# Optimization experiments

Measured on AMD Instinct MI355X. Metric: run time of the kernel, lower is better.

## Reference

```python
import jax, jax.numpy as jnp
import numpy as np

N_POINTS = 32768
N_PRIMS = 2048
C_LIGHT = 299792458.0


def setup_inputs() -> dict:
    key = jax.random.key(0)
    k1, k2, k3, k4, k5 = jax.random.split(key, 5)
    # query points and primitive centers in a ~room-scale scene (metres)
    query_points = jax.random.normal(k1, (N_POINTS, 3), dtype=jnp.float32) * 2.0
    positions = jax.random.normal(k2, (N_PRIMS, 3), dtype=jnp.float32) * 2.0
    # diagonal anisotropic scales, kept away from zero for stability
    scales = jax.random.uniform(k3, (N_PRIMS, 3), dtype=jnp.float32, minval=0.1, maxval=1.0)
    amplitudes = jax.random.uniform(k4, (N_PRIMS,), dtype=jnp.float32, minval=0.0, maxval=1.0)
    phases = jax.random.uniform(k5, (N_PRIMS,), dtype=jnp.float32, minval=-np.pi, maxval=np.pi)
    return {
        "query_points": query_points,
        "positions": positions,
        "scales": scales,
        "amplitudes": amplitudes,
        "phases": phases,
        "frequency": 2400000000,  # 2.4 GHz
    }


def reference(query_points, positions, scales, amplitudes, phases, frequency):
    """Batched equivalent of: field = sum_p primitive_p.evaluate(query_points, frequency).

    Each complex Gaussian primitive contributes
        a_p * exp(-0.5 * (x-mu_p)^T diag(1/s_p^2) (x-mu_p)) * exp(i*(phi_p + k*|x-mu_p|))
    with wavenumber k = 2*pi*f/c. All pairwise terms are expressed as GEMMs.
    """
    f = jnp.float32(frequency)
    k_wave = jnp.float32(2.0 * np.pi) * f / jnp.float32(C_LIGHT)

    inv_var = 1.0 / (scales * scales)                      # [P,3]
    x2 = query_points * query_points                       # [N,3]
    mu2w = jnp.sum(positions * positions * inv_var, axis=1)  # [P]
    # Mahalanobis distance^2: sum_d (x_d-mu_d)^2 / s_d^2, expanded into GEMMs
    maha = (x2 @ inv_var.T
            - 2.0 * (query_points @ (positions * inv_var).T)
            + mu2w[None, :])                               # [N,P]
    maha = jnp.maximum(maha, 0.0)
    # Euclidean distance for the propagation phase
    d2 = (jnp.sum(x2, axis=1, keepdims=True)
          - 2.0 * (query_points @ positions.T)
          + jnp.sum(positions * positions, axis=1)[None, :])  # [N,P]
    r = jnp.sqrt(jnp.maximum(d2, 1e-12))

    w = amplitudes[None, :] * jnp.exp(-0.5 * maha)         # [N,P] real envelope
    ph = phases[None, :] + k_wave * r                      # [N,P] total phase
    field = jax.lax.complex(jnp.sum(w * jnp.cos(ph), axis=1),
                            jnp.sum(w * jnp.sin(ph), axis=1))  # [N] complex64
    return field
```

## Files before the change

### kernel.cpp

```cpp
#include <hip/hip_runtime.h>
#include <math.h>

#define NPOINTS 32768
#define NPRIMS  2048
#define BLK     256

typedef float v2f __attribute__((ext_vector_type(2)));

struct PrimDup { float4 q0, q1, q2, q3; };

__device__ __forceinline__ float read_freq(const void* p) {
    const unsigned* w = (const unsigned*)p;
    unsigned lo = w[0];
    float ff = __uint_as_float(lo);
    if (ff >= 1.0e5f && ff <= 1.0e13f) return ff;
    if (lo != 0u) return (float)lo;
    double d = *(const double*)p;
    if (d >= 1.0e5 && d <= 1.0e13) return (float)d;
    unsigned long long v = ((unsigned long long)w[1] << 32) | lo;
    return (float)v;
}

__global__ __launch_bounds__(BLK) void prep_kernel(
        const float* __restrict__ pos,
        const float* __restrict__ scl,
        const float* __restrict__ amp,
        const float* __restrict__ ph,
        PrimDup* __restrict__ pd) {
    int p = blockIdx.x * blockDim.x + threadIdx.x;
    if (p >= NPRIMS) return;
    const float KE     = -0.72134752044448169f;
    const float INV2PI =  0.15915494309189535f;
    float sx = scl[3*p+0], sy = scl[3*p+1], sz = scl[3*p+2];
    float gx = KE / (sx*sx), gy = KE / (sy*sy), gz = KE / (sz*sz);
    float pr = ph[p] * INV2PI;
    PrimDup D;
    D.q0 = make_float4(pos[3*p+0], pos[3*p+0], pos[3*p+1], pos[3*p+1]);
    D.q1 = make_float4(pos[3*p+2], pos[3*p+2], amp[p], amp[p]);
    D.q2 = make_float4(gx, gx, gy, gy);
    D.q3 = make_float4(gz, gz, pr, pr);
    pd[p] = D;
}

template <int NSPLIT>
__global__ __launch_bounds__(BLK) void field_kernel(
        const float* __restrict__ qp,
        const PrimDup* __restrict__ pd,
        const void* __restrict__ freq_p,
        float2* __restrict__ part) {
    constexpr int PCOUNT = NPRIMS / NSPLIT;
    const int n0 = blockIdx.x * (BLK * 2) + threadIdx.x;
    const int n1 = n0 + BLK;
    const float kr = read_freq(freq_p) / 299792458.0f;
    const v2f kr2 = {kr, kr};

    const v2f xx = {qp[3*n0+0], qp[3*n1+0]};
    const v2f yy = {qp[3*n0+1], qp[3*n1+1]};
    const v2f zz = {qp[3*n0+2], qp[3*n1+2]};

    v2f re = {0.0f, 0.0f}, im = {0.0f, 0.0f};

    const int base = blockIdx.y * PCOUNT;
    #pragma unroll 4
    for (int j = 0; j < PCOUNT; ++j) {
        PrimDup D = pd[base + j];
        v2f mux = {D.q0.x, D.q0.y}, muy = {D.q0.z, D.q0.w};
        v2f muz = {D.q1.x, D.q1.y}, am2 = {D.q1.z, D.q1.w};
        v2f gx  = {D.q2.x, D.q2.y}, gy  = {D.q2.z, D.q2.w};
        v2f gz  = {D.q3.x, D.q3.y}, ph2 = {D.q3.z, D.q3.w};

        v2f dx = xx - mux, dy = yy - muy, dz = zz - muz;
        v2f t0 = dx * dx, t1 = dy * dy, t2 = dz * dz;
        v2f e  = t0 * gx + t1 * gy + t2 * gz;
        v2f d2 = t0 + t1 + t2;
        d2 = __builtin_elementwise_max(d2, (v2f){1e-12f, 1e-12f});

        v2f r2 = {__builtin_amdgcn_sqrtf(d2.x), __builtin_amdgcn_sqrtf(d2.y)};
        v2f ex = {__builtin_amdgcn_exp2f(e.x),  __builtin_amdgcn_exp2f(e.y)};
        v2f w2 = am2 * ex;
        v2f tp = __builtin_elementwise_fma(kr2, r2, ph2);
        float f0 = __builtin_amdgcn_fractf(tp.x);
        float f1 = __builtin_amdgcn_fractf(tp.y);
        v2f s2 = {__builtin_amdgcn_sinf(f0), __builtin_amdgcn_sinf(f1)};
        v2f c2 = {__builtin_amdgcn_cosf(f0), __builtin_amdgcn_cosf(f1)};
        re = __builtin_elementwise_fma(w2, c2, re);
        im = __builtin_elementwise_fma(w2, s2, im);
    }

    part[(size_t)blockIdx.y * NPOINTS + n0] = make_float2(re.x, im.x);
    part[(size_t)blockIdx.y * NPOINTS + n1] = make_float2(re.y, im.y);
}

template <int NSPLIT>
__global__ __launch_bounds__(BLK) void reduce_kernel(const float2* __restrict__ part,
                                                     float* __restrict__ out) {
    int n = blockIdx.x * blockDim.x + threadIdx.x;
    float re = 0.0f, im = 0.0f;
    #pragma unroll
    for (int s = 0; s < NSPLIT; ++s) {
        float2 v = part[(size_t)s * NPOINTS + n];
        re += v.x; im += v.y;
    }
    out[n]           = re;
    out[NPOINTS + n] = im;
}

__global__ __launch_bounds__(BLK) void field_fallback(
        const float* __restrict__ qp,
        const float* __restrict__ pos,
        const float* __restrict__ scl,
        const float* __restrict__ amp,
        const float* __restrict__ ph,
        const void*  __restrict__ freq_p,
        float*       __restrict__ out) {
    __shared__ float4 sA[128];
    __shared__ float4 sB[128];
    const int n = blockIdx.x * BLK + threadIdx.x;
    const float x = qp[3*n+0], y = qp[3*n+1], z = qp[3*n+2];
    const float kr = read_freq(freq_p) / 299792458.0f;
    const float KE = -0.72134752044448169f, INV2PI = 0.15915494309189535f;
    float re = 0.0f, im = 0.0f;
    for (int tile = 0; tile < NPRIMS / 128; ++tile) {
        __syncthreads();
        if (threadIdx.x < 128) {
            int p = tile * 128 + threadIdx.x;
            float sx = scl[3*p+0], sy = scl[3*p+1], sz = scl[3*p+2];
            sA[threadIdx.x] = make_float4(pos[3*p+0], pos[3*p+1], pos[3*p+2], amp[p]);
            sB[threadIdx.x] = make_float4(KE/(sx*sx), KE/(sy*sy), KE/(sz*sz), ph[p]*INV2PI);
        }
        __syncthreads();
        #pragma unroll 8
        for (int p = 0; p < 128; ++p) {
            float4 a = sA[p];
            float4 b = sB[p];
            float dx = x - a.x, dy = y - a.y, dz = z - a.z;
            float t0 = dx*dx, t1 = dy*dy, t2 = dz*dz;
            float e  = fmaf(t0, b.x, fmaf(t1, b.y, t2 * b.z));
            float d2 = t0 + t1 + t2;
            float r  = __builtin_amdgcn_sqrtf(fmaxf(d2, 1e-12f));
            float w  = a.w * __builtin_amdgcn_exp2f(e);
            float tp = __builtin_amdgcn_fractf(fmaf(kr, r, b.w));
            float s  = __builtin_amdgcn_sinf(tp);
            float c  = __builtin_amdgcn_cosf(tp);
            re = fmaf(w, c, re);
            im = fmaf(w, s, im);
        }
    }
    out[n]           = re;
    out[NPOINTS + n] = im;
}

extern "C" void kernel_launch(void* const* d_in, const int* in_sizes, int n_in,
                              void* d_out, int out_size, void* d_ws, size_t ws_size,
                              hipStream_t stream) {
    const float* qp  = (const float*)d_in[0];
    const float* pos = (const float*)d_in[1];
    const float* scl = (const float*)d_in[2];
    const float* amp = (const float*)d_in[3];
    const float* ph  = (const float*)d_in[4];
    const void*  fq  = d_in[5];
    float* out = (float*)d_out;

    const size_t packed_bytes = (size_t)NPRIMS * sizeof(PrimDup);
    const size_t ps32 = packed_bytes + (size_t)32 * NPOINTS * sizeof(float2);
    const size_t ps16 = packed_bytes + (size_t)16 * NPOINTS * sizeof(float2);

    if (ws_size >= ps32) {
        PrimDup* pd   = (PrimDup*)d_ws;
        float2*  part = (float2*)((char*)d_ws + packed_bytes);
        prep_kernel<<<dim3(NPRIMS / BLK), dim3(BLK), 0, stream>>>(pos, scl, amp, ph, pd);
        field_kernel<32><<<dim3(NPOINTS / (BLK * 2), 32), dim3(BLK), 0, stream>>>(qp, pd, fq, part);
        reduce_kernel<32><<<dim3(NPOINTS / BLK), dim3(BLK), 0, stream>>>(part, out);
    } else if (ws_size >= ps16) {
        PrimDup* pd   = (PrimDup*)d_ws;
        float2*  part = (float2*)((char*)d_ws + packed_bytes);
        prep_kernel<<<dim3(NPRIMS / BLK), dim3(BLK), 0, stream>>>(pos, scl, amp, ph, pd);
        field_kernel<16><<<dim3(NPOINTS / (BLK * 2), 16), dim3(BLK), 0, stream>>>(qp, pd, fq, part);
        reduce_kernel<16><<<dim3(NPOINTS / BLK), dim3(BLK), 0, stream>>>(part, out);
    } else {
        field_fallback<<<dim3(NPOINTS / BLK), dim3(BLK), 0, stream>>>(qp, pos, scl, amp, ph, fq, out);
    }
}
```

Measured before the change: 50.74 us.

## Process four points per thread and split primitives 64 ways

Each thread now evaluates two packed point pairs, so every loaded primitive record is reused across four query points instead of two. The primitive dimension is split into 64 chunks instead of 32 to keep the grid size constant. In exchange, the partial-sum buffer and the reduction pass double in size, and the path needs a larger workspace.

```diff
diff --git a/kernel.cpp b/kernel.cpp
--- a/kernel.cpp
+++ b/kernel.cpp
@@ -42,26 +42,31 @@
     pd[p] = D;
 }
 
-template <int NSPLIT>
+template <int NSPLIT, int NPAIR>
 __global__ __launch_bounds__(BLK) void field_kernel(
         const float* __restrict__ qp,
         const PrimDup* __restrict__ pd,
         const void* __restrict__ freq_p,
         float2* __restrict__ part) {
     constexpr int PCOUNT = NPRIMS / NSPLIT;
-    const int n0 = blockIdx.x * (BLK * 2) + threadIdx.x;
-    const int n1 = n0 + BLK;
+    const int n0 = blockIdx.x * (BLK * 2 * NPAIR) + threadIdx.x;
     const float kr = read_freq(freq_p) / 299792458.0f;
     const v2f kr2 = {kr, kr};
 
-    const v2f xx = {qp[3*n0+0], qp[3*n1+0]};
-    const v2f yy = {qp[3*n0+1], qp[3*n1+1]};
-    const v2f zz = {qp[3*n0+2], qp[3*n1+2]};
-
-    v2f re = {0.0f, 0.0f}, im = {0.0f, 0.0f};
+    v2f xx[NPAIR], yy[NPAIR], zz[NPAIR], re[NPAIR], im[NPAIR];
+    #pragma unroll
+    for (int i = 0; i < NPAIR; ++i) {
+        int a = n0 + (2 * i) * BLK;
+        int b = n0 + (2 * i + 1) * BLK;
+        xx[i] = (v2f){qp[3*a+0], qp[3*b+0]};
+        yy[i] = (v2f){qp[3*a+1], qp[3*b+1]};
+        zz[i] = (v2f){qp[3*a+2], qp[3*b+2]};
+        re[i] = (v2f){0.0f, 0.0f};
+        im[i] = (v2f){0.0f, 0.0f};
+    }
 
     const int base = blockIdx.y * PCOUNT;
-    #pragma unroll 4
+    #pragma unroll 2
     for (int j = 0; j < PCOUNT; ++j) {
         PrimDup D = pd[base + j];
         v2f mux = {D.q0.x, D.q0.y}, muy = {D.q0.z, D.q0.w};
@@ -69,26 +74,34 @@
         v2f gx  = {D.q2.x, D.q2.y}, gy  = {D.q2.z, D.q2.w};
         v2f gz  = {D.q3.x, D.q3.y}, ph2 = {D.q3.z, D.q3.w};
 
-        v2f dx = xx - mux, dy = yy - muy, dz = zz - muz;
-        v2f t0 = dx * dx, t1 = dy * dy, t2 = dz * dz;
-        v2f e  = t0 * gx + t1 * gy + t2 * gz;
-        v2f d2 = t0 + t1 + t2;
-        d2 = __builtin_elementwise_max(d2, (v2f){1e-12f, 1e-12f});
+        #pragma unroll
+        for (int i = 0; i < NPAIR; ++i) {
+            v2f dx = xx[i] - mux, dy = yy[i] - muy, dz = zz[i] - muz;
+            v2f t0 = dx * dx, t1 = dy * dy, t2 = dz * dz;
+            v2f e  = t0 * gx + t1 * gy + t2 * gz;
+            v2f d2 = t0 + t1 + t2;
+            d2 = __builtin_elementwise_max(d2, (v2f){1e-12f, 1e-12f});
 
-        v2f r2 = {__builtin_amdgcn_sqrtf(d2.x), __builtin_amdgcn_sqrtf(d2.y)};
-        v2f ex = {__builtin_amdgcn_exp2f(e.x),  __builtin_amdgcn_exp2f(e.y)};
-        v2f w2 = am2 * ex;
-        v2f tp = __builtin_elementwise_fma(kr2, r2, ph2);
-        float f0 = __builtin_amdgcn_fractf(tp.x);
-        float f1 = __builtin_amdgcn_fractf(tp.y);
-        v2f s2 = {__builtin_amdgcn_sinf(f0), __builtin_amdgcn_sinf(f1)};
-        v2f c2 = {__builtin_amdgcn_cosf(f0), __builtin_amdgcn_cosf(f1)};
-        re = __builtin_elementwise_fma(w2, c2, re);
-        im = __builtin_elementwise_fma(w2, s2, im);
+            v2f r2 = {__builtin_amdgcn_sqrtf(d2.x), __builtin_amdgcn_sqrtf(d2.y)};
+            v2f ex = {__builtin_amdgcn_exp2f(e.x),  __builtin_amdgcn_exp2f(e.y)};
+            v2f w2 = am2 * ex;
+            v2f tp = __builtin_elementwise_fma(kr2, r2, ph2);
+            float f0 = __builtin_amdgcn_fractf(tp.x);
+            float f1 = __builtin_amdgcn_fractf(tp.y);
+            v2f s2 = {__builtin_amdgcn_sinf(f0), __builtin_amdgcn_sinf(f1)};
+            v2f c2 = {__builtin_amdgcn_cosf(f0), __builtin_amdgcn_cosf(f1)};
+            re[i] = __builtin_elementwise_fma(w2, c2, re[i]);
+            im[i] = __builtin_elementwise_fma(w2, s2, im[i]);
+        }
     }
 
-    part[(size_t)blockIdx.y * NPOINTS + n0] = make_float2(re.x, im.x);
-    part[(size_t)blockIdx.y * NPOINTS + n1] = make_float2(re.y, im.y);
+    #pragma unroll
+    for (int i = 0; i < NPAIR; ++i) {
+        int a = n0 + (2 * i) * BLK;
+        int b = n0 + (2 * i + 1) * BLK;
+        part[(size_t)blockIdx.y * NPOINTS + a] = make_float2(re[i].x, im[i].x);
+        part[(size_t)blockIdx.y * NPOINTS + b] = make_float2(re[i].y, im[i].y);
+    }
 }
 
 template <int NSPLIT>
@@ -162,21 +175,21 @@
     float* out = (float*)d_out;
 
     const size_t packed_bytes = (size_t)NPRIMS * sizeof(PrimDup);
+    const size_t ps64 = packed_bytes + (size_t)64 * NPOINTS * sizeof(float2);
     const size_t ps32 = packed_bytes + (size_t)32 * NPOINTS * sizeof(float2);
-    const size_t ps16 = packed_bytes + (size_t)16 * NPOINTS * sizeof(float2);
 
-    if (ws_size >= ps32) {
+    if (ws_size >= ps64) {
         PrimDup* pd   = (PrimDup*)d_ws;
         float2*  part = (float2*)((char*)d_ws + packed_bytes);
         prep_kernel<<<dim3(NPRIMS / BLK), dim3(BLK), 0, stream>>>(pos, scl, amp, ph, pd);
-        field_kernel<32><<<dim3(NPOINTS / (BLK * 2), 32), dim3(BLK), 0, stream>>>(qp, pd, fq, part);
-        reduce_kernel<32><<<dim3(NPOINTS / BLK), dim3(BLK), 0, stream>>>(part, out);
-    } else if (ws_size >= ps16) {
+        field_kernel<64, 2><<<dim3(NPOINTS / (BLK * 4), 64), dim3(BLK), 0, stream>>>(qp, pd, fq, part);
+        reduce_kernel<64><<<dim3(NPOINTS / BLK), dim3(BLK), 0, stream>>>(part, out);
+    } else if (ws_size >= ps32) {
         PrimDup* pd   = (PrimDup*)d_ws;
         float2*  part = (float2*)((char*)d_ws + packed_bytes);
         prep_kernel<<<dim3(NPRIMS / BLK), dim3(BLK), 0, stream>>>(pos, scl, amp, ph, pd);
-        field_kernel<16><<<dim3(NPOINTS / (BLK * 2), 16), dim3(BLK), 0, stream>>>(qp, pd, fq, part);
-        reduce_kernel<16><<<dim3(NPOINTS / BLK), dim3(BLK), 0, stream>>>(part, out);
+        field_kernel<32, 1><<<dim3(NPOINTS / (BLK * 2), 32), dim3(BLK), 0, stream>>>(qp, pd, fq, part);
+        reduce_kernel<32><<<dim3(NPOINTS / BLK), dim3(BLK), 0, stream>>>(part, out);
     } else {
         field_fallback<<<dim3(NPOINTS / BLK), dim3(BLK), 0, stream>>>(qp, pos, scl, amp, ph, fq, out);
     }
```

New measurement: 55.85 us. +10.1%, slower.

## Spatially sort query points and cull negligible Gaussian primitives per wavefront

Applied to the files above, without the earlier changes.

Adds a Morton-cell binning pipeline (histogram, scan, scatter) that reorders query points so each wavefront covers a compact region. In the field kernel each wavefront computes a bounding box of its points and skips any primitive whose Gaussian exponent over that box is provably below 2^-21. Skipped primitives contribute at most that tiny relative weight, so the heavy transcendental work drops for distant primitives. The cost is five extra small kernel launches, atomics, an indirect scatter on output, and a small approximation error.

```diff
diff --git a/kernel.cpp b/kernel.cpp
--- a/kernel.cpp
+++ b/kernel.cpp
@@ -4,6 +4,7 @@
 #define NPOINTS 32768
 #define NPRIMS  2048
 #define BLK     256
+#define NCELLS  4096
 
 typedef float v2f __attribute__((ext_vector_type(2)));
 
@@ -22,44 +23,174 @@
 }
 
 __global__ __launch_bounds__(BLK) void prep_kernel(
-        const float* __restrict__ pos,
-        const float* __restrict__ scl,
-        const float* __restrict__ amp,
-        const float* __restrict__ ph,
+        const float* __restrict__ pos, const float* __restrict__ scl,
+        const float* __restrict__ amp, const float* __restrict__ ph,
         PrimDup* __restrict__ pd) {
     int p = blockIdx.x * blockDim.x + threadIdx.x;
     if (p >= NPRIMS) return;
-    const float KE     = -0.72134752044448169f;
-    const float INV2PI =  0.15915494309189535f;
+    const float KE = -0.72134752044448169f, INV2PI = 0.15915494309189535f;
     float sx = scl[3*p+0], sy = scl[3*p+1], sz = scl[3*p+2];
-    float gx = KE / (sx*sx), gy = KE / (sy*sy), gz = KE / (sz*sz);
-    float pr = ph[p] * INV2PI;
     PrimDup D;
     D.q0 = make_float4(pos[3*p+0], pos[3*p+0], pos[3*p+1], pos[3*p+1]);
     D.q1 = make_float4(pos[3*p+2], pos[3*p+2], amp[p], amp[p]);
-    D.q2 = make_float4(gx, gx, gy, gy);
-    D.q3 = make_float4(gz, gz, pr, pr);
+    D.q2 = make_float4(KE/(sx*sx), KE/(sx*sx), KE/(sy*sy), KE/(sy*sy));
+    D.q3 = make_float4(KE/(sz*sz), KE/(sz*sz), ph[p]*INV2PI, ph[p]*INV2PI);
     pd[p] = D;
 }
 
+__device__ __forceinline__ unsigned sp4(unsigned b) {
+    return (b & 1u) | ((b & 2u) << 2) | ((b & 4u) << 4) | ((b & 8u) << 6);
+}
+__device__ __forceinline__ unsigned cell_of(float x, float y, float z) {
+    int qx = (int)((x + 6.4f) * 1.25f); qx = qx < 0 ? 0 : (qx > 15 ? 15 : qx);
+    int qy = (int)((y + 6.4f) * 1.25f); qy = qy < 0 ? 0 : (qy > 15 ? 15 : qy);
+    int qz = (int)((z + 6.4f) * 1.25f); qz = qz < 0 ? 0 : (qz > 15 ? 15 : qz);
+    return sp4((unsigned)qx) | (sp4((unsigned)qy) << 1) | (sp4((unsigned)qz) << 2);
+}
+
+__global__ __launch_bounds__(BLK) void zero_hist(unsigned* __restrict__ hist) {
+    int i = blockIdx.x * blockDim.x + threadIdx.x;
+    if (i < NCELLS) hist[i] = 0;
+}
+
+__global__ __launch_bounds__(BLK) void hist_kernel(
+        const float* __restrict__ qp, unsigned* __restrict__ hist,
+        unsigned* __restrict__ cellid) {
+    int n = blockIdx.x * blockDim.x + threadIdx.x;
+    unsigned c = cell_of(qp[3*n+0], qp[3*n+1], qp[3*n+2]);
+    cellid[n] = c;
+    atomicAdd(&hist[c], 1u);
+}
+
+__global__ __launch_bounds__(BLK) void scan_kernel(unsigned* __restrict__ hist) {
+    __shared__ unsigned tot[BLK];
+    const int t = threadIdx.x;
+    unsigned loc[16]; unsigned s = 0;
+    #pragma unroll
+    for (int i = 0; i < 16; ++i) { loc[i] = hist[t*16 + i]; s += loc[i]; }
+    tot[t] = s;
+    __syncthreads();
+    for (int off = 1; off < BLK; off <<= 1) {
+        unsigned u = (t >= off) ? tot[t - off] : 0u;
+        __syncthreads();
+        tot[t] += u;
+        __syncthreads();
+    }
+    unsigned run = tot[t] - s;
+    #pragma unroll
+    for (int i = 0; i < 16; ++i) { hist[t*16 + i] = run; run += loc[i]; }
+}
+
+__global__ __launch_bounds__(BLK) void scatter_kernel(
+        const float* __restrict__ qp, const unsigned* __restrict__ cellid,
+        unsigned* __restrict__ off, float4* __restrict__ sxyz,
+        unsigned* __restrict__ sidx) {
+    int n = blockIdx.x * blockDim.x + threadIdx.x;
+    unsigned pos = atomicAdd(&off[cellid[n]], 1u);
+    sxyz[pos] = make_float4(qp[3*n+0], qp[3*n+1], qp[3*n+2], 0.0f);
+    sidx[pos] = (unsigned)n;
+}
+
 template <int NSPLIT>
-__global__ __launch_bounds__(BLK) void field_kernel(
-        const float* __restrict__ qp,
+__global__ __launch_bounds__(BLK) void field_sorted(
+        const float4* __restrict__ sxyz,
         const PrimDup* __restrict__ pd,
         const void* __restrict__ freq_p,
         float2* __restrict__ part) {
+    constexpr int PCOUNT = NPRIMS / NSPLIT;
+    const int lane = threadIdx.x & 63;
+    const int wid  = threadIdx.x >> 6;
+    const int base = blockIdx.x * (BLK * 2) + wid * 128;
+    const int i0 = base + lane, i1 = base + 64 + lane;
+
+    const float4 p0 = sxyz[i0], p1 = sxyz[i1];
+    const float kr = read_freq(freq_p) / 299792458.0f;
+    const v2f kr2 = {kr, kr};
+    const v2f xx = {p0.x, p1.x}, yy = {p0.y, p1.y}, zz = {p0.z, p1.z};
+
+    float mnx = fminf(p0.x, p1.x), mxx = fmaxf(p0.x, p1.x);
+    float mny = fminf(p0.y, p1.y), mxy = fmaxf(p0.y, p1.y);
+    float mnz = fminf(p0.z, p1.z), mxz = fmaxf(p0.z, p1.z);
+    #pragma unroll
+    for (int m = 1; m < 64; m <<= 1) {
+        mnx = fminf(mnx, __shfl_xor(mnx, m, 64));
+        mxx = fmaxf(mxx, __shfl_xor(mxx, m, 64));
+        mny = fminf(mny, __shfl_xor(mny, m, 64));
+        mxy = fmaxf(mxy, __shfl_xor(mxy, m, 64));
+        mnz = fminf(mnz, __shfl_xor(mnz, m, 64));
+        mxz = fmaxf(mxz, __shfl_xor(mxz, m, 64));
+    }
+    const float cx = 0.5f*(mnx+mxx), ex = 0.5f*(mxx-mnx);
+    const float cy = 0.5f*(mny+mxy), ey = 0.5f*(mxy-mny);
+    const float cz = 0.5f*(mnz+mxz), ez = 0.5f*(mxz-mnz);
+
+    v2f re = {0.0f, 0.0f}, im = {0.0f, 0.0f};
+    const int pb = blockIdx.y * PCOUNT;
+    #pragma unroll 2
+    for (int j = 0; j < PCOUNT; ++j) {
+        PrimDup D = pd[pb + j];
+        float tx = fmaxf(fabsf(cx - D.q0.x) - ex, 0.0f);
+        float ty = fmaxf(fabsf(cy - D.q0.z) - ey, 0.0f);
+        float tz = fmaxf(fabsf(cz - D.q1.x) - ez, 0.0f);
+        float bound = tx*tx*D.q2.x + ty*ty*D.q2.z + tz*tz*D.q3.x;
+        if (bound > -21.0f) {
+            v2f mux = {D.q0.x, D.q0.y}, muy = {D.q0.z, D.q0.w};
+            v2f muz = {D.q1.x, D.q1.y}, am2 = {D.q1.z, D.q1.w};
+            v2f gx  = {D.q2.x, D.q2.y}, gy  = {D.q2.z, D.q2.w};
+            v2f gz  = {D.q3.x, D.q3.y}, ph2 = {D.q3.z, D.q3.w};
+
+            v2f dx = xx - mux, dy = yy - muy, dz = zz - muz;
+            v2f t0 = dx * dx, t1 = dy * dy, t2 = dz * dz;
+            v2f e  = t0 * gx + t1 * gy + t2 * gz;
+            v2f d2 = t0 + t1 + t2;
+            d2 = __builtin_elementwise_max(d2, (v2f){1e-12f, 1e-12f});
+
+            v2f r2 = {__builtin_amdgcn_sqrtf(d2.x), __builtin_amdgcn_sqrtf(d2.y)};
+            v2f exw = {__builtin_amdgcn_exp2f(e.x), __builtin_amdgcn_exp2f(e.y)};
+            v2f w2 = am2 * exw;
+            v2f tp = __builtin_elementwise_fma(kr2, r2, ph2);
+            float f0 = __builtin_amdgcn_fractf(tp.x);
+            float f1 = __builtin_amdgcn_fractf(tp.y);
+            v2f s2 = {__builtin_amdgcn_sinf(f0), __builtin_amdgcn_sinf(f1)};
+            v2f c2 = {__builtin_amdgcn_cosf(f0), __builtin_amdgcn_cosf(f1)};
+            re = __builtin_elementwise_fma(w2, c2, re);
+            im = __builtin_elementwise_fma(w2, s2, im);
+        }
+    }
+
+    part[(size_t)blockIdx.y * NPOINTS + i0] = make_float2(re.x, im.x);
+    part[(size_t)blockIdx.y * NPOINTS + i1] = make_float2(re.y, im.y);
+}
+
+template <int NSPLIT>
+__global__ __launch_bounds__(BLK) void reduce_sorted(
+        const float2* __restrict__ part, const unsigned* __restrict__ sidx,
+        float* __restrict__ out) {
+    int pos = blockIdx.x * blockDim.x + threadIdx.x;
+    float re = 0.0f, im = 0.0f;
+    #pragma unroll
+    for (int s = 0; s < NSPLIT; ++s) {
+        float2 v = part[(size_t)s * NPOINTS + pos];
+        re += v.x; im += v.y;
+    }
+    unsigned n = sidx[pos];
+    out[n]           = re;
+    out[NPOINTS + n] = im;
+}
+
+template <int NSPLIT>
+__global__ __launch_bounds__(BLK) void field_kernel(
+        const float* __restrict__ qp, const PrimDup* __restrict__ pd,
+        const void* __restrict__ freq_p, float2* __restrict__ part) {
     constexpr int PCOUNT = NPRIMS / NSPLIT;
     const int n0 = blockIdx.x * (BLK * 2) + threadIdx.x;
     const int n1 = n0 + BLK;
     const float kr = read_freq(freq_p) / 299792458.0f;
     const v2f kr2 = {kr, kr};
-
     const v2f xx = {qp[3*n0+0], qp[3*n1+0]};
     const v2f yy = {qp[3*n0+1], qp[3*n1+1]};
     const v2f zz = {qp[3*n0+2], qp[3*n1+2]};
-
     v2f re = {0.0f, 0.0f}, im = {0.0f, 0.0f};
-
     const int base = blockIdx.y * PCOUNT;
     #pragma unroll 4
     for (int j = 0; j < PCOUNT; ++j) {
@@ -68,13 +199,11 @@
         v2f muz = {D.q1.x, D.q1.y}, am2 = {D.q1.z, D.q1.w};
         v2f gx  = {D.q2.x, D.q2.y}, gy  = {D.q2.z, D.q2.w};
         v2f gz  = {D.q3.x, D.q3.y}, ph2 = {D.q3.z, D.q3.w};
-
         v2f dx = xx - mux, dy = yy - muy, dz = zz - muz;
         v2f t0 = dx * dx, t1 = dy * dy, t2 = dz * dz;
         v2f e  = t0 * gx + t1 * gy + t2 * gz;
         v2f d2 = t0 + t1 + t2;
         d2 = __builtin_elementwise_max(d2, (v2f){1e-12f, 1e-12f});
-
         v2f r2 = {__builtin_amdgcn_sqrtf(d2.x), __builtin_amdgcn_sqrtf(d2.y)};
         v2f ex = {__builtin_amdgcn_exp2f(e.x),  __builtin_amdgcn_exp2f(e.y)};
         v2f w2 = am2 * ex;
@@ -86,7 +215,6 @@
         re = __builtin_elementwise_fma(w2, c2, re);
         im = __builtin_elementwise_fma(w2, s2, im);
     }
-
     part[(size_t)blockIdx.y * NPOINTS + n0] = make_float2(re.x, im.x);
     part[(size_t)blockIdx.y * NPOINTS + n1] = make_float2(re.y, im.y);
 }
@@ -106,13 +234,10 @@
 }
 
 __global__ __launch_bounds__(BLK) void field_fallback(
-        const float* __restrict__ qp,
-        const float* __restrict__ pos,
-        const float* __restrict__ scl,
-        const float* __restrict__ amp,
-        const float* __restrict__ ph,
-        const void*  __restrict__ freq_p,
-        float*       __restrict__ out) {
+        const float* __restrict__ qp, const float* __restrict__ pos,
+        const float* __restrict__ scl, const float* __restrict__ amp,
+        const float* __restrict__ ph, const void* __restrict__ freq_p,
+        float* __restrict__ out) {
     __shared__ float4 sA[128];
     __shared__ float4 sB[128];
     const int n = blockIdx.x * BLK + threadIdx.x;
@@ -131,8 +256,7 @@
         __syncthreads();
         #pragma unroll 8
         for (int p = 0; p < 128; ++p) {
-            float4 a = sA[p];
-            float4 b = sB[p];
+            float4 a = sA[p]; float4 b = sB[p];
             float dx = x - a.x, dy = y - a.y, dz = z - a.z;
             float t0 = dx*dx, t1 = dy*dy, t2 = dz*dz;
             float e  = fmaf(t0, b.x, fmaf(t1, b.y, t2 * b.z));
@@ -161,22 +285,37 @@
     const void*  fq  = d_in[5];
     float* out = (float*)d_out;
 
-    const size_t packed_bytes = (size_t)NPRIMS * sizeof(PrimDup);
-    const size_t ps32 = packed_bytes + (size_t)32 * NPOINTS * sizeof(float2);
-    const size_t ps16 = packed_bytes + (size_t)16 * NPOINTS * sizeof(float2);
-
-    if (ws_size >= ps32) {
+    const size_t pd_b   = (size_t)NPRIMS * sizeof(PrimDup);
+    const size_t hist_b = (size_t)NCELLS * 4;
+    const size_t cid_b  = (size_t)NPOINTS * 4;
+    const size_t sxyz_b = (size_t)NPOINTS * 16;
+    const size_t sidx_b = (size_t)NPOINTS * 4;
+    const size_t head   = pd_b + hist_b + cid_b + sxyz_b + sidx_b;
+    const size_t sorted_need = head + (size_t)32 * NPOINTS * sizeof(float2);
+    const size_t r10_need = pd_b + (size_t)32 * NPOINTS * sizeof(float2);
+
+    if (ws_size >= sorted_need) {
+        char* w = (char*)d_ws;
+        PrimDup*  pd   = (PrimDup*)w;                 w += pd_b;
+        unsigned* hist = (unsigned*)w;                w += hist_b;
+        unsigned* cid  = (unsigned*)w;                w += cid_b;
+        float4*   sxyz = (float4*)w;                  w += sxyz_b;
+        unsigned* sidx = (unsigned*)w;                w += sidx_b;
+        float2*   part = (float2*)w;
+
+        prep_kernel<<<dim3(NPRIMS / BLK), dim3(BLK), 0, stream>>>(pos, scl, amp, ph, pd);
+        zero_hist<<<dim3(NCELLS / BLK), dim3(BLK), 0, stream>>>(hist);
+        hist_kernel<<<dim3(NPOINTS / BLK), dim3(BLK), 0, stream>>>(qp, hist, cid);
+        scan_kernel<<<dim3(1), dim3(BLK), 0, stream>>>(hist);
+        scatter_kernel<<<dim3(NPOINTS / BLK), dim3(BLK), 0, stream>>>(qp, cid, hist, sxyz, sidx);
+        field_sorted<32><<<dim3(NPOINTS / (BLK * 2), 32), dim3(BLK), 0, stream>>>(sxyz, pd, fq, part);
+        reduce_sorted<32><<<dim3(NPOINTS / BLK), dim3(BLK), 0, stream>>>(part, sidx, out);
+    } else if (ws_size >= r10_need) {
         PrimDup* pd   = (PrimDup*)d_ws;
-        float2*  part = (float2*)((char*)d_ws + packed_bytes);
+        float2*  part = (float2*)((char*)d_ws + pd_b);
         prep_kernel<<<dim3(NPRIMS / BLK), dim3(BLK), 0, stream>>>(pos, scl, amp, ph, pd);
         field_kernel<32><<<dim3(NPOINTS / (BLK * 2), 32), dim3(BLK), 0, stream>>>(qp, pd, fq, part);
         reduce_kernel<32><<<dim3(NPOINTS / BLK), dim3(BLK), 0, stream>>>(part, out);
-    } else if (ws_size >= ps16) {
-        PrimDup* pd   = (PrimDup*)d_ws;
-        float2*  part = (float2*)((char*)d_ws + packed_bytes);
-        prep_kernel<<<dim3(NPRIMS / BLK), dim3(BLK), 0, stream>>>(pos, scl, amp, ph, pd);
-        field_kernel<16><<<dim3(NPOINTS / (BLK * 2), 16), dim3(BLK), 0, stream>>>(qp, pd, fq, part);
-        reduce_kernel<16><<<dim3(NPOINTS / BLK), dim3(BLK), 0, stream>>>(part, out);
     } else {
         field_fallback<<<dim3(NPOINTS / BLK), dim3(BLK), 0, stream>>>(qp, pos, scl, amp, ph, fq, out);
     }
```

After: 79.98 us. 1.58x slower.
